# Optimization experiments

Hardware: AMD Instinct MI355X
Metric: run time of the kernel (lower is better)

Reference implementation:

```python
import jax, jax.numpy as jnp
import numpy as np

N_NODES = 50000
IN_CH = 32
HID = 64
N_EDGES = 800000
B = 4


def setup_inputs() -> dict:
    key = jax.random.key(0)
    ks = jax.random.split(key, 20)
    inp = {
        "x": jax.random.normal(ks[0], (B, N_NODES, IN_CH), dtype=jnp.float32),
        "h": jax.random.normal(ks[1], (B, N_NODES, HID), dtype=jnp.float32),
        "edge_index": jax.random.randint(ks[2], (2, N_EDGES), 0, N_NODES, dtype=jnp.int64),
        "edge_weight": jax.random.uniform(ks[3], (N_EDGES,), dtype=jnp.float32),
    }
    # 6 GCNConv layers: uz, hz, ur, hr, uh, hh. W stored as [in, out]; bias [out].
    names = [("uz", IN_CH), ("hz", HID), ("ur", IN_CH), ("hr", HID), ("uh", IN_CH), ("hh", HID)]
    for i, (nm, cin) in enumerate(names):
        scale = 1.0 / np.sqrt(cin)
        inp[f"W_{nm}"] = jax.random.uniform(ks[4 + 2 * i], (cin, HID), minval=-scale, maxval=scale, dtype=jnp.float32)
        inp[f"b_{nm}"] = jax.random.uniform(ks[5 + 2 * i], (HID,), minval=-scale, maxval=scale, dtype=jnp.float32)
    return inp


def _gcn_norm(edge_index, edge_weight, n):
    # add self-loops with weight 1, symmetric normalization (PyG GCNConv default)
    loop = jnp.arange(n, dtype=edge_index.dtype)
    src = jnp.concatenate([edge_index[0], loop])
    dst = jnp.concatenate([edge_index[1], loop])
    w = jnp.concatenate([edge_weight, jnp.ones((n,), edge_weight.dtype)])
    deg = jnp.zeros((n,), edge_weight.dtype).at[dst].add(w)
    dinv = jnp.where(deg > 0, jax.lax.rsqrt(jnp.maximum(deg, 1e-12)), 0.0)
    norm = dinv[src] * w * dinv[dst]
    return src, dst, norm


def _gcn(x, W, b, src, dst, norm, n):
    # x: [B, N, Cin] -> [B, N, H]; linear then normalized scatter-add over edges
    xw = jnp.einsum("bnc,ch->bnh", x, W)
    msg = xw[:, src, :] * norm[None, :, None]          # [B, E+N, H]
    agg = jnp.zeros((x.shape[0], n, W.shape[1]), x.dtype).at[:, dst].add(msg)
    return agg + b


def reference(x, h, edge_index, edge_weight,
              W_uz, b_uz, W_hz, b_hz, W_ur, b_ur, W_hr, b_hr, W_uh, b_uh, W_hh, b_hh):
    n = x.shape[1]
    src, dst, norm = _gcn_norm(edge_index, edge_weight, n)
    z = jax.nn.sigmoid(_gcn(x, W_uz, b_uz, src, dst, norm, n)
                       + _gcn(h, W_hz, b_hz, src, dst, norm, n))
    r = jax.nn.sigmoid(_gcn(x, W_ur, b_ur, src, dst, norm, n)
                       + _gcn(h, W_hr, b_hr, src, dst, norm, n))
    h_hat = jnp.tanh(_gcn(x, W_uh, b_uh, src, dst, norm, n)
                     + _gcn(r * h, W_hh, b_hh, src, dst, norm, n))
    return (1.0 - z) * h + z * h_hat
```

## Files before the change

### kernel.cpp

```cpp
#include <hip/hip_runtime.h>
#include <math.h>

#define NN 50000
#define CIN 32
#define HD  64
#define NE  800000
#define NB  4
#define NBLK 196
#define NTILE 12500
#define TPB   3125
#define DWAVES 2048

typedef unsigned int uint32;
typedef unsigned short ushort_t;
typedef unsigned long long u64;
typedef __attribute__((ext_vector_type(8))) short bf16x8;
typedef __attribute__((ext_vector_type(4))) float f32x4;

__device__ __forceinline__ uint32 pk2(float a, float b) {
    uint32 ua = __float_as_uint(a), ub = __float_as_uint(b);
    uint32 ra = (ua + 0x7FFFu + ((ua >> 16) & 1u)) >> 16;
    uint32 rb = (ub + 0x7FFFu + ((ub >> 16) & 1u)) >> 16;
    return ra | (rb << 16);
}
__device__ __forceinline__ ushort_t b1(float v) {
    uint32 u = __float_as_uint(v);
    return (ushort_t)((u + 0x7FFFu + ((u >> 16) & 1u)) >> 16);
}
__device__ __forceinline__ float ub(ushort_t v) {
    return __uint_as_float(((uint32)v) << 16);
}
__device__ __forceinline__ float blo(uint32 v) { return __uint_as_float(v << 16); }
__device__ __forceinline__ float bhi(uint32 v) { return __uint_as_float(v & 0xFFFF0000u); }
__device__ __forceinline__ float sigm(float v) { return 1.0f / (1.0f + __expf(-v)); }


__global__ void k_prep(const float* __restrict__ x, const float* __restrict__ h,
                       const float* __restrict__ Wuz, const float* __restrict__ Whz,
                       const float* __restrict__ Wur, const float* __restrict__ Whr,
                       const float* __restrict__ Wuh, const float* __restrict__ Whh,
                       const float* __restrict__ buz, const float* __restrict__ bhz,
                       const float* __restrict__ bur, const float* __restrict__ bhr,
                       const float* __restrict__ buh, const float* __restrict__ bhh,
                       uint32* __restrict__ F, u64* __restrict__ degcnt,
                       uint32* __restrict__ WB, float* __restrict__ BS) {
    int stride = gridDim.x * blockDim.x;
    int tid = blockIdx.x * blockDim.x + threadIdx.x;

    if (tid < NN) degcnt[tid] = (1ull << 24);

    if (tid < 9216) {
        int g = tid / 3072, rem = tid - g * 3072;
        int kt = rem >> 10, r2 = rem & 1023;
        int ct = r2 >> 8, r3 = r2 & 255;
        int l = r3 >> 2, jp = r3 & 3;
        int k = kt * 32 + ((l >> 4) << 3) + 2 * jp;
        int ch = ct * 16 + (l & 15);
        const float* Wu = (g == 0) ? Wuz : (g == 1) ? Wur : Wuh;
        const float* Wh = (g == 0) ? Whz : (g == 1) ? Whr : Whh;
        float w0 = (k < 32) ? Wu[k * 64 + ch] : Wh[(k - 32) * 64 + ch];
        int k1 = k + 1;
        float w1 = (k1 < 32) ? Wu[k1 * 64 + ch] : Wh[(k1 - 32) * 64 + ch];
        WB[tid] = pk2(w0, w1);
    }
    if (tid < 192) {
        int g = tid >> 6, c = tid & 63;
        const float* bu = (g == 0) ? buz : (g == 1) ? bur : buh;
        const float* bh = (g == 0) ? bhz : (g == 1) ? bhr : bhh;
        BS[tid] = bu[c] + bh[c];
    }

    for (int t = tid; t < NB * NN * (CIN / 2); t += stride) {
        int cp = t & 15; int rest = t >> 4;
        int b = rest / NN; int n = rest - b * NN;
        float2 v = *(const float2*)&x[(b * NN + n) * CIN + 2 * cp];
        F[n * 192 + b * 16 + cp] = pk2(v.x, v.y);
    }
    for (int t = tid; t < NB * NN * (HD / 2); t += stride) {
        int cp = t & 31; int rest = t >> 5;
        int b = rest / NN; int n = rest - b * NN;
        float2 v = *(const float2*)&h[(b * NN + n) * HD + 2 * cp];
        F[n * 192 + 64 + b * 32 + cp] = pk2(v.x, v.y);
    }
}

__global__ void k_degcnt(const int* __restrict__ ei, const float* __restrict__ ew,
                         u64* __restrict__ degcnt) {
    int stride = gridDim.x * blockDim.x;
    for (int e = blockIdx.x * blockDim.x + threadIdx.x; e < NE; e += stride) {
        int d = ei[NE + e];
        u64 val = (1ull << 40) + (u64)(uint32)(ew[e] * 16777216.0f + 0.5f);
        atomicAdd(&degcnt[d], val);
    }
}


__global__ void k_scan1(const u64* __restrict__ degcnt, int* __restrict__ tmp,
                        int* __restrict__ partials) {
    __shared__ int lds[256];
    int i = blockIdx.x * 256 + threadIdx.x;
    int v = (i < NN) ? (int)(degcnt[i] >> 40) : 0;
    lds[threadIdx.x] = v;
    __syncthreads();
    for (int off = 1; off < 256; off <<= 1) {
        int t = (threadIdx.x >= off) ? lds[threadIdx.x - off] : 0;
        __syncthreads();
        lds[threadIdx.x] += t;
        __syncthreads();
    }
    if (i < NN) tmp[i] = lds[threadIdx.x];
    if (threadIdx.x == 255) partials[blockIdx.x] = lds[255];
}

__global__ void k_scan2(int* __restrict__ partials) {
    __shared__ int lds[256];
    int v = (threadIdx.x < NBLK) ? partials[threadIdx.x] : 0;
    lds[threadIdx.x] = v;
    __syncthreads();
    for (int off = 1; off < 256; off <<= 1) {
        int t = (threadIdx.x >= off) ? lds[threadIdx.x - off] : 0;
        __syncthreads();
        lds[threadIdx.x] += t;
        __syncthreads();
    }
    int ex = (threadIdx.x > 0) ? lds[threadIdx.x - 1] : 0;
    if (threadIdx.x < NBLK) partials[threadIdx.x] = ex;
}

__global__ void k_scan3(const int* __restrict__ tmp, const u64* __restrict__ degcnt,
                        const int* __restrict__ partials,
                        int* __restrict__ rowptr, int* __restrict__ cursor,
                        float* __restrict__ dinv) {
    int i = blockIdx.x * blockDim.x + threadIdx.x;
    if (i < NN) {
        u64 dc = degcnt[i];
        int cnt = (int)(dc >> 40);
        int inc = tmp[i] + partials[i >> 8];
        rowptr[i + 1] = inc;
        cursor[i] = inc - cnt;
        if (i == 0) rowptr[0] = 0;
        float dg = (float)(dc & 0xFFFFFFFFFFull) * 5.9604644775390625e-08f;
        dinv[i] = (dg > 0.0f) ? rsqrtf(fmaxf(dg, 1e-12f)) : 0.0f;
    }
}

__global__ void k_bucket(const int* __restrict__ ei, const float* __restrict__ ew,
                         const float* __restrict__ dinv,
                         int* __restrict__ cursor, int2* __restrict__ eb) {
    int stride = gridDim.x * blockDim.x;
    for (int e = blockIdx.x * blockDim.x + threadIdx.x; e < NE; e += stride) {
        int s = ei[e], d = ei[NE + e];
        float nrm = dinv[s] * ew[e] * dinv[d];
        int pos = atomicAdd(&cursor[d], 1);
        eb[pos] = make_int2(s, __float_as_int(nrm));
    }
}


__global__ __launch_bounds__(256) void k_gather_xh(
    const int* __restrict__ rowptr, const int2* __restrict__ eb,
    const float* __restrict__ dinv, const uint32* __restrict__ F,
    uint32* __restrict__ AggU) {

    int l = threadIdx.x & 63;
    int d = __builtin_amdgcn_readfirstlane(blockIdx.x * 4 + (threadIdx.x >> 6));
    float dv = dinv[d];
    float s2 = dv * dv;

    const uint32* fp = F + 3 * l;
    const uint32* sp = fp + d * 192;
    uint32 u0 = sp[0], u1 = sp[1], u2 = sp[2];
    float a0 = s2 * blo(u0), a1 = s2 * bhi(u0);
    float a2 = s2 * blo(u1), a3 = s2 * bhi(u1);
    float a4 = s2 * blo(u2), a5 = s2 * bhi(u2);

    int e  = rowptr[d];
    int e1 = rowptr[d + 1];

    for (; e + 7 < e1; e += 8) {
        int2 p0 = eb[e],     p1 = eb[e + 1], p2 = eb[e + 2], p3 = eb[e + 3];
        int2 p4 = eb[e + 4], p5 = eb[e + 5], p6 = eb[e + 6], p7 = eb[e + 7];
        const uint32* q0 = fp + p0.x * 192;
        const uint32* q1 = fp + p1.x * 192;
        const uint32* q2 = fp + p2.x * 192;
        const uint32* q3 = fp + p3.x * 192;
        const uint32* q4 = fp + p4.x * 192;
        const uint32* q5 = fp + p5.x * 192;
        const uint32* q6 = fp + p6.x * 192;
        const uint32* q7 = fp + p7.x * 192;
        uint32 v00 = q0[0], v01 = q0[1], v02 = q0[2];
        uint32 v10 = q1[0], v11 = q1[1], v12 = q1[2];
        uint32 v20 = q2[0], v21 = q2[1], v22 = q2[2];
        uint32 v30 = q3[0], v31 = q3[1], v32 = q3[2];
        uint32 v40 = q4[0], v41 = q4[1], v42 = q4[2];
        uint32 v50 = q5[0], v51 = q5[1], v52 = q5[2];
        uint32 v60 = q6[0], v61 = q6[1], v62 = q6[2];
        uint32 v70 = q7[0], v71 = q7[1], v72 = q7[2];
        float n0 = __int_as_float(p0.y), n1 = __int_as_float(p1.y);
        float n2 = __int_as_float(p2.y), n3 = __int_as_float(p3.y);
        float n4 = __int_as_float(p4.y), n5 = __int_as_float(p5.y);
        float n6 = __int_as_float(p6.y), n7 = __int_as_float(p7.y);
        a0 = fmaf(n0, blo(v00), a0); a1 = fmaf(n0, bhi(v00), a1);
        a2 = fmaf(n0, blo(v01), a2); a3 = fmaf(n0, bhi(v01), a3);
        a4 = fmaf(n0, blo(v02), a4); a5 = fmaf(n0, bhi(v02), a5);
        a0 = fmaf(n1, blo(v10), a0); a1 = fmaf(n1, bhi(v10), a1);
        a2 = fmaf(n1, blo(v11), a2); a3 = fmaf(n1, bhi(v11), a3);
        a4 = fmaf(n1, blo(v12), a4); a5 = fmaf(n1, bhi(v12), a5);
        a0 = fmaf(n2, blo(v20), a0); a1 = fmaf(n2, bhi(v20), a1);
        a2 = fmaf(n2, blo(v21), a2); a3 = fmaf(n2, bhi(v21), a3);
        a4 = fmaf(n2, blo(v22), a4); a5 = fmaf(n2, bhi(v22), a5);
        a0 = fmaf(n3, blo(v30), a0); a1 = fmaf(n3, bhi(v30), a1);
        a2 = fmaf(n3, blo(v31), a2); a3 = fmaf(n3, bhi(v31), a3);
        a4 = fmaf(n3, blo(v32), a4); a5 = fmaf(n3, bhi(v32), a5);
        a0 = fmaf(n4, blo(v40), a0); a1 = fmaf(n4, bhi(v40), a1);
        a2 = fmaf(n4, blo(v41), a2); a3 = fmaf(n4, bhi(v41), a3);
        a4 = fmaf(n4, blo(v42), a4); a5 = fmaf(n4, bhi(v42), a5);
        a0 = fmaf(n5, blo(v50), a0); a1 = fmaf(n5, bhi(v50), a1);
        a2 = fmaf(n5, blo(v51), a2); a3 = fmaf(n5, bhi(v51), a3);
        a4 = fmaf(n5, blo(v52), a4); a5 = fmaf(n5, bhi(v52), a5);
        a0 = fmaf(n6, blo(v60), a0); a1 = fmaf(n6, bhi(v60), a1);
        a2 = fmaf(n6, blo(v61), a2); a3 = fmaf(n6, bhi(v61), a3);
        a4 = fmaf(n6, blo(v62), a4); a5 = fmaf(n6, bhi(v62), a5);
        a0 = fmaf(n7, blo(v70), a0); a1 = fmaf(n7, bhi(v70), a1);
        a2 = fmaf(n7, blo(v71), a2); a3 = fmaf(n7, bhi(v71), a3);
        a4 = fmaf(n7, blo(v72), a4); a5 = fmaf(n7, bhi(v72), a5);
    }
    for (; e + 3 < e1; e += 4) {
        int2 p0 = eb[e], p1 = eb[e + 1], p2 = eb[e + 2], p3 = eb[e + 3];
        const uint32* q0 = fp + p0.x * 192;
        const uint32* q1 = fp + p1.x * 192;
        const uint32* q2 = fp + p2.x * 192;
        const uint32* q3 = fp + p3.x * 192;
        uint32 v00 = q0[0], v01 = q0[1], v02 = q0[2];
        uint32 v10 = q1[0], v11 = q1[1], v12 = q1[2];
        uint32 v20 = q2[0], v21 = q2[1], v22 = q2[2];
        uint32 v30 = q3[0], v31 = q3[1], v32 = q3[2];
        float n0 = __int_as_float(p0.y), n1 = __int_as_float(p1.y);
        float n2 = __int_as_float(p2.y), n3 = __int_as_float(p3.y);
        a0 = fmaf(n0, blo(v00), a0); a1 = fmaf(n0, bhi(v00), a1);
        a2 = fmaf(n0, blo(v01), a2); a3 = fmaf(n0, bhi(v01), a3);
        a4 = fmaf(n0, blo(v02), a4); a5 = fmaf(n0, bhi(v02), a5);
        a0 = fmaf(n1, blo(v10), a0); a1 = fmaf(n1, bhi(v10), a1);
        a2 = fmaf(n1, blo(v11), a2); a3 = fmaf(n1, bhi(v11), a3);
        a4 = fmaf(n1, blo(v12), a4); a5 = fmaf(n1, bhi(v12), a5);
        a0 = fmaf(n2, blo(v20), a0); a1 = fmaf(n2, bhi(v20), a1);
        a2 = fmaf(n2, blo(v21), a2); a3 = fmaf(n2, bhi(v21), a3);
        a4 = fmaf(n2, blo(v22), a4); a5 = fmaf(n2, bhi(v22), a5);
        a0 = fmaf(n3, blo(v30), a0); a1 = fmaf(n3, bhi(v30), a1);
        a2 = fmaf(n3, blo(v31), a2); a3 = fmaf(n3, bhi(v31), a3);
        a4 = fmaf(n3, blo(v32), a4); a5 = fmaf(n3, bhi(v32), a5);
    }
    for (; e < e1; ++e) {
        int2 p0 = eb[e];
        const uint32* q0 = fp + p0.x * 192;
        uint32 v00 = q0[0], v01 = q0[1], v02 = q0[2];
        float n0 = __int_as_float(p0.y);
        a0 = fmaf(n0, blo(v00), a0); a1 = fmaf(n0, bhi(v00), a1);
        a2 = fmaf(n0, blo(v01), a2); a3 = fmaf(n0, bhi(v01), a3);
        a4 = fmaf(n0, blo(v02), a4); a5 = fmaf(n0, bhi(v02), a5);
    }

    uint32* op = AggU + d * 192 + 3 * l;
    op[0] = pk2(a0, a1);
    op[1] = pk2(a2, a3);
    op[2] = pk2(a4, a5);
}

__global__ __launch_bounds__(256) void k_gather_rh(
    const int* __restrict__ rowptr, const int2* __restrict__ eb,
    const float* __restrict__ dinv, const uint32* __restrict__ R,
    uint32* __restrict__ AggU) {

    int l = threadIdx.x & 63;
    int d = __builtin_amdgcn_readfirstlane(blockIdx.x * 4 + (threadIdx.x >> 6));
    float dv = dinv[d];
    float s2 = dv * dv;

    const uint32* rp = R + 2 * l;
    uint2 sv = *(const uint2*)(rp + d * 128);
    float a0 = s2 * blo(sv.x), a1 = s2 * bhi(sv.x);
    float a2 = s2 * blo(sv.y), a3 = s2 * bhi(sv.y);

    int e  = rowptr[d];
    int e1 = rowptr[d + 1];

    for (; e + 7 < e1; e += 8) {
        int2 p0 = eb[e],     p1 = eb[e + 1], p2 = eb[e + 2], p3 = eb[e + 3];
        int2 p4 = eb[e + 4], p5 = eb[e + 5], p6 = eb[e + 6], p7 = eb[e + 7];
        uint2 v0 = *(const uint2*)(rp + p0.x * 128);
        uint2 v1 = *(const uint2*)(rp + p1.x * 128);
        uint2 v2 = *(const uint2*)(rp + p2.x * 128);
        uint2 v3 = *(const uint2*)(rp + p3.x * 128);
        uint2 v4 = *(const uint2*)(rp + p4.x * 128);
        uint2 v5 = *(const uint2*)(rp + p5.x * 128);
        uint2 v6 = *(const uint2*)(rp + p6.x * 128);
        uint2 v7 = *(const uint2*)(rp + p7.x * 128);
        float n0 = __int_as_float(p0.y), n1 = __int_as_float(p1.y);
        float n2 = __int_as_float(p2.y), n3 = __int_as_float(p3.y);
        float n4 = __int_as_float(p4.y), n5 = __int_as_float(p5.y);
        float n6 = __int_as_float(p6.y), n7 = __int_as_float(p7.y);
        a0 = fmaf(n0, blo(v0.x), a0); a1 = fmaf(n0, bhi(v0.x), a1);
        a2 = fmaf(n0, blo(v0.y), a2); a3 = fmaf(n0, bhi(v0.y), a3);
        a0 = fmaf(n1, blo(v1.x), a0); a1 = fmaf(n1, bhi(v1.x), a1);
        a2 = fmaf(n1, blo(v1.y), a2); a3 = fmaf(n1, bhi(v1.y), a3);
        a0 = fmaf(n2, blo(v2.x), a0); a1 = fmaf(n2, bhi(v2.x), a1);
        a2 = fmaf(n2, blo(v2.y), a2); a3 = fmaf(n2, bhi(v2.y), a3);
        a0 = fmaf(n3, blo(v3.x), a0); a1 = fmaf(n3, bhi(v3.x), a1);
        a2 = fmaf(n3, blo(v3.y), a2); a3 = fmaf(n3, bhi(v3.y), a3);
        a0 = fmaf(n4, blo(v4.x), a0); a1 = fmaf(n4, bhi(v4.x), a1);
        a2 = fmaf(n4, blo(v4.y), a2); a3 = fmaf(n4, bhi(v4.y), a3);
        a0 = fmaf(n5, blo(v5.x), a0); a1 = fmaf(n5, bhi(v5.x), a1);
        a2 = fmaf(n5, blo(v5.y), a2); a3 = fmaf(n5, bhi(v5.y), a3);
        a0 = fmaf(n6, blo(v6.x), a0); a1 = fmaf(n6, bhi(v6.x), a1);
        a2 = fmaf(n6, blo(v6.y), a2); a3 = fmaf(n6, bhi(v6.y), a3);
        a0 = fmaf(n7, blo(v7.x), a0); a1 = fmaf(n7, bhi(v7.x), a1);
        a2 = fmaf(n7, blo(v7.y), a2); a3 = fmaf(n7, bhi(v7.y), a3);
    }
    for (; e + 3 < e1; e += 4) {
        int2 p0 = eb[e], p1 = eb[e + 1], p2 = eb[e + 2], p3 = eb[e + 3];
        uint2 v0 = *(const uint2*)(rp + p0.x * 128);
        uint2 v1 = *(const uint2*)(rp + p1.x * 128);
        uint2 v2 = *(const uint2*)(rp + p2.x * 128);
        uint2 v3 = *(const uint2*)(rp + p3.x * 128);
        float n0 = __int_as_float(p0.y), n1 = __int_as_float(p1.y);
        float n2 = __int_as_float(p2.y), n3 = __int_as_float(p3.y);
        a0 = fmaf(n0, blo(v0.x), a0); a1 = fmaf(n0, bhi(v0.x), a1);
        a2 = fmaf(n0, blo(v0.y), a2); a3 = fmaf(n0, bhi(v0.y), a3);
        a0 = fmaf(n1, blo(v1.x), a0); a1 = fmaf(n1, bhi(v1.x), a1);
        a2 = fmaf(n1, blo(v1.y), a2); a3 = fmaf(n1, bhi(v1.y), a3);
        a0 = fmaf(n2, blo(v2.x), a0); a1 = fmaf(n2, bhi(v2.x), a1);
        a2 = fmaf(n2, blo(v2.y), a2); a3 = fmaf(n2, bhi(v2.y), a3);
        a0 = fmaf(n3, blo(v3.x), a0); a1 = fmaf(n3, bhi(v3.x), a1);
        a2 = fmaf(n3, blo(v3.y), a2); a3 = fmaf(n3, bhi(v3.y), a3);
    }
    for (; e < e1; ++e) {
        int2 p0 = eb[e];
        uint2 v0 = *(const uint2*)(rp + p0.x * 128);
        float n0 = __int_as_float(p0.y);
        a0 = fmaf(n0, blo(v0.x), a0); a1 = fmaf(n0, bhi(v0.x), a1);
        a2 = fmaf(n0, blo(v0.y), a2); a3 = fmaf(n0, bhi(v0.y), a3);
    }

    *(uint2*)&AggU[d * 192 + 64 + (l >> 4) * 32 + ((2 * l) & 31)] =
        make_uint2(pk2(a0, a1), pk2(a2, a3));
}


__global__ __launch_bounds__(256) void k_zr(
    const uint32* __restrict__ AggU, const float* __restrict__ h,
    const uint32* __restrict__ WB, const float* __restrict__ BS,
    ushort_t* __restrict__ Zb, ushort_t* __restrict__ R16) {

    int l  = threadIdx.x & 63;
    int wv = blockIdx.x * 4 + (threadIdx.x >> 6);
    int lr = l & 15, lg = l >> 4;

    const bf16x8* wz = (const bf16x8*)WB;
    const bf16x8* wr = (const bf16x8*)(WB + 3072);
    bf16x8 wzf[12], wrf[12];
    #pragma unroll
    for (int f = 0; f < 12; ++f) { wzf[f] = wz[f * 64 + l]; wrf[f] = wr[f * 64 + l]; }
    float bz[4], br[4];
    #pragma unroll
    for (int ct = 0; ct < 4; ++ct) {
        bz[ct] = BS[ct * 16 + lr];
        br[ct] = BS[64 + ct * 16 + lr];
    }

    for (int t = wv; t < NTILE; t += DWAVES) {
        int bb = t / TPB, nt = t - bb * TPB;
        const uint32* base = AggU + (nt * 16 + lr) * 192;
        bf16x8 af0 = *(const bf16x8*)(base + bb * 16 + lg * 4);
        bf16x8 af1 = *(const bf16x8*)(base + 64 + bb * 32 + lg * 4);
        bf16x8 af2 = *(const bf16x8*)(base + 64 + bb * 32 + 16 + lg * 4);

        f32x4 az[4], ar[4];
        #pragma unroll
        for (int c = 0; c < 4; ++c) { az[c] = (f32x4){0,0,0,0}; ar[c] = (f32x4){0,0,0,0}; }

        #pragma unroll
        for (int ct = 0; ct < 4; ++ct) {
            az[ct] = __builtin_amdgcn_mfma_f32_16x16x32_bf16(af0, wzf[0*4+ct], az[ct], 0,0,0);
            ar[ct] = __builtin_amdgcn_mfma_f32_16x16x32_bf16(af0, wrf[0*4+ct], ar[ct], 0,0,0);
            az[ct] = __builtin_amdgcn_mfma_f32_16x16x32_bf16(af1, wzf[1*4+ct], az[ct], 0,0,0);
            ar[ct] = __builtin_amdgcn_mfma_f32_16x16x32_bf16(af1, wrf[1*4+ct], ar[ct], 0,0,0);
            az[ct] = __builtin_amdgcn_mfma_f32_16x16x32_bf16(af2, wzf[2*4+ct], az[ct], 0,0,0);
            ar[ct] = __builtin_amdgcn_mfma_f32_16x16x32_bf16(af2, wrf[2*4+ct], ar[ct], 0,0,0);
        }

        int node0 = nt * 16;
        #pragma unroll
        for (int ct = 0; ct < 4; ++ct) {
            int ch = ct * 16 + lr;
            #pragma unroll
            for (int rr = 0; rr < 4; ++rr) {
                int node = node0 + lg * 4 + rr;
                int off  = (bb * NN + node) * 64 + ch;
                float zv = sigm(az[ct][rr] + bz[ct]);
                float rv = sigm(ar[ct][rr] + br[ct]);
                float hv = h[off];
                Zb[off] = b1(zv);
                R16[node * 256 + bb * 64 + ch] = b1(rv * hv);
            }
        }
    }
}

__global__ __launch_bounds__(256) void k_final(
    const uint32* __restrict__ AggU, const float* __restrict__ h,
    const uint32* __restrict__ WB, const float* __restrict__ BS,
    const ushort_t* __restrict__ Zb, float* __restrict__ out) {

    int l  = threadIdx.x & 63;
    int wv = blockIdx.x * 4 + (threadIdx.x >> 6);
    int lr = l & 15, lg = l >> 4;

    const bf16x8* wh = (const bf16x8*)(WB + 6144);
    bf16x8 whf[12];
    #pragma unroll
    for (int f = 0; f < 12; ++f) whf[f] = wh[f * 64 + l];
    float bs[4];
    #pragma unroll
    for (int ct = 0; ct < 4; ++ct) bs[ct] = BS[128 + ct * 16 + lr];

    for (int t = wv; t < NTILE; t += DWAVES) {
        int bb = t / TPB, nt = t - bb * TPB;
        const uint32* base = AggU + (nt * 16 + lr) * 192;
        bf16x8 af0 = *(const bf16x8*)(base + bb * 16 + lg * 4);
        bf16x8 af1 = *(const bf16x8*)(base + 64 + bb * 32 + lg * 4);
        bf16x8 af2 = *(const bf16x8*)(base + 64 + bb * 32 + 16 + lg * 4);

        f32x4 ac[4];
        #pragma unroll
        for (int c = 0; c < 4; ++c) ac[c] = (f32x4){0,0,0,0};

        #pragma unroll
        for (int ct = 0; ct < 4; ++ct) {
            ac[ct] = __builtin_amdgcn_mfma_f32_16x16x32_bf16(af0, whf[0*4+ct], ac[ct], 0,0,0);
            ac[ct] = __builtin_amdgcn_mfma_f32_16x16x32_bf16(af1, whf[1*4+ct], ac[ct], 0,0,0);
            ac[ct] = __builtin_amdgcn_mfma_f32_16x16x32_bf16(af2, whf[2*4+ct], ac[ct], 0,0,0);
        }

        int node0 = nt * 16;
        #pragma unroll
        for (int ct = 0; ct < 4; ++ct) {
            int ch = ct * 16 + lr;
            #pragma unroll
            for (int rr = 0; rr < 4; ++rr) {
                int node = node0 + lg * 4 + rr;
                int off  = (bb * NN + node) * 64 + ch;
                float hh = tanhf(ac[ct][rr] + bs[ct]);
                float zv = ub(Zb[off]);
                float hv = h[off];
                out[off] = (1.0f - zv) * hv + zv * hh;
            }
        }
    }
}


extern "C" void kernel_launch(void* const* d_in, const int* in_sizes, int n_in,
                              void* d_out, int out_size, void* d_ws, size_t ws_size,
                              hipStream_t stream) {
    const float* x   = (const float*)d_in[0];
    const float* h   = (const float*)d_in[1];
    const int*   ei  = (const int*)d_in[2];
    const float* ew  = (const float*)d_in[3];
    const float* Wuz = (const float*)d_in[4];
    const float* buz = (const float*)d_in[5];
    const float* Whz = (const float*)d_in[6];
    const float* bhz = (const float*)d_in[7];
    const float* Wur = (const float*)d_in[8];
    const float* bur = (const float*)d_in[9];
    const float* Whr = (const float*)d_in[10];
    const float* bhr = (const float*)d_in[11];
    const float* Wuh = (const float*)d_in[12];
    const float* buh = (const float*)d_in[13];
    const float* Whh = (const float*)d_in[14];
    const float* bhh = (const float*)d_in[15];
    float* out = (float*)d_out;

    float*    w      = (float*)d_ws;
    u64*      degcnt = (u64*)w;
    float*    dinv   = w + 102400;
    int*      rowptr = (int*)(w + 153600);
    int2*     eb     = (int2*)(w + 204800);
    uint32*   F      = (uint32*)(w + 1804800);
    uint32*   R      = F;
    uint32*   AggU   = (uint32*)(w + 11404800);
    ushort_t* Zb     = (ushort_t*)(w + 21004800);
    uint32*   WB     = (uint32*)(w + 27404800);
    float*    BS     = (float*)(w + 27414016);
    int*      tmp    = (int*)(w + 27414208);
    int*      cursor = (int*)(w + 27465408);
    int*      parts  = (int*)(w + 27516608);

    k_prep<<<2048, 256, 0, stream>>>(x, h,
                                     Wuz, Whz, Wur, Whr, Wuh, Whh,
                                     buz, bhz, bur, bhr, buh, bhh,
                                     F, degcnt, WB, BS);
    k_degcnt<<<2048, 256, 0, stream>>>(ei, ew, degcnt);

    k_scan1<<<NBLK, 256, 0, stream>>>(degcnt, tmp, parts);
    k_scan2<<<1, 256, 0, stream>>>(parts);
    k_scan3<<<NBLK, 256, 0, stream>>>(tmp, degcnt, parts, rowptr, cursor, dinv);

    k_bucket<<<2048, 256, 0, stream>>>(ei, ew, dinv, cursor, eb);

    k_gather_xh<<<NN / 4, 256, 0, stream>>>(rowptr, eb, dinv, F, AggU);

    k_zr<<<DWAVES / 4, 256, 0, stream>>>(AggU, h, WB, BS, Zb, (ushort_t*)R);

    k_gather_rh<<<NN / 4, 256, 0, stream>>>(rowptr, eb, dinv, R, AggU);

    k_final<<<DWAVES / 4, 256, 0, stream>>>(AggU, h, WB, BS, Zb, out);
}
```

Baseline: 350.7 us.

## Vectorize prep packing, store Z in MFMA fragment order, read bf16 h copy

The prep kernel now reads x and h as float4 and writes two packed bf16 pairs per store. The z/r and final kernels read h from the bf16 packed feature buffer instead of fp32 global h, halving those reads. Z is stored as uint2 in the MFMA output-fragment order, so each lane writes and reads it with one 8-byte access instead of scattered 2-byte ones. The workspace is re-laid out so R no longer aliases F, because F must survive until k_final; using bf16 h in the final blend adds rounding error to the output.

```diff
diff --git a/kernel.cpp b/kernel.cpp
--- a/kernel.cpp
+++ b/kernel.cpp
@@ -23,26 +23,19 @@
     uint32 rb = (ub + 0x7FFFu + ((ub >> 16) & 1u)) >> 16;
     return ra | (rb << 16);
 }
-__device__ __forceinline__ ushort_t b1(float v) {
-    uint32 u = __float_as_uint(v);
-    return (ushort_t)((u + 0x7FFFu + ((u >> 16) & 1u)) >> 16);
-}
-__device__ __forceinline__ float ub(ushort_t v) {
-    return __uint_as_float(((uint32)v) << 16);
-}
 __device__ __forceinline__ float blo(uint32 v) { return __uint_as_float(v << 16); }
 __device__ __forceinline__ float bhi(uint32 v) { return __uint_as_float(v & 0xFFFF0000u); }
 __device__ __forceinline__ float sigm(float v) { return 1.0f / (1.0f + __expf(-v)); }
 
 
-__global__ void k_prep(const float* __restrict__ x, const float* __restrict__ h,
+__global__ void k_prep(const float4* __restrict__ x4, const float4* __restrict__ h4,
                        const float* __restrict__ Wuz, const float* __restrict__ Whz,
                        const float* __restrict__ Wur, const float* __restrict__ Whr,
                        const float* __restrict__ Wuh, const float* __restrict__ Whh,
                        const float* __restrict__ buz, const float* __restrict__ bhz,
                        const float* __restrict__ bur, const float* __restrict__ bhr,
                        const float* __restrict__ buh, const float* __restrict__ bhh,
-                       uint32* __restrict__ F, u64* __restrict__ degcnt,
+                       uint2* __restrict__ F2, u64* __restrict__ degcnt,
                        uint32* __restrict__ WB, float* __restrict__ BS) {
     int stride = gridDim.x * blockDim.x;
     int tid = blockIdx.x * blockDim.x + threadIdx.x;
@@ -70,17 +63,17 @@
         BS[tid] = bu[c] + bh[c];
     }
 
-    for (int t = tid; t < NB * NN * (CIN / 2); t += stride) {
-        int cp = t & 15; int rest = t >> 4;
+    for (int t = tid; t < NB * NN * (CIN / 4); t += stride) {
+        int cq = t & 7; int rest = t >> 3;
         int b = rest / NN; int n = rest - b * NN;
-        float2 v = *(const float2*)&x[(b * NN + n) * CIN + 2 * cp];
-        F[n * 192 + b * 16 + cp] = pk2(v.x, v.y);
-    }
-    for (int t = tid; t < NB * NN * (HD / 2); t += stride) {
-        int cp = t & 31; int rest = t >> 5;
+        float4 v = x4[(b * NN + n) * 8 + cq];
+        F2[n * 96 + b * 8 + cq] = make_uint2(pk2(v.x, v.y), pk2(v.z, v.w));
+    }
+    for (int t = tid; t < NB * NN * (HD / 4); t += stride) {
+        int cq = t & 15; int rest = t >> 4;
         int b = rest / NN; int n = rest - b * NN;
-        float2 v = *(const float2*)&h[(b * NN + n) * HD + 2 * cp];
-        F[n * 192 + 64 + b * 32 + cp] = pk2(v.x, v.y);
+        float4 v = h4[(b * NN + n) * 16 + cq];
+        F2[n * 96 + 32 + b * 16 + cq] = make_uint2(pk2(v.x, v.y), pk2(v.z, v.w));
     }
 }
 
@@ -347,9 +340,9 @@
 
 
 __global__ __launch_bounds__(256) void k_zr(
-    const uint32* __restrict__ AggU, const float* __restrict__ h,
+    const uint32* __restrict__ AggU, const uint32* __restrict__ F,
     const uint32* __restrict__ WB, const float* __restrict__ BS,
-    ushort_t* __restrict__ Zb, ushort_t* __restrict__ R16) {
+    uint2* __restrict__ Zb2, ushort_t* __restrict__ R16) {
 
     int l  = threadIdx.x & 63;
     int wv = blockIdx.x * 4 + (threadIdx.x >> 6);
@@ -392,24 +385,33 @@
         #pragma unroll
         for (int ct = 0; ct < 4; ++ct) {
             int ch = ct * 16 + lr;
+            uint32 z01, z23;
             #pragma unroll
             for (int rr = 0; rr < 4; ++rr) {
                 int node = node0 + lg * 4 + rr;
-                int off  = (bb * NN + node) * 64 + ch;
                 float zv = sigm(az[ct][rr] + bz[ct]);
                 float rv = sigm(ar[ct][rr] + br[ct]);
-                float hv = h[off];
-                Zb[off] = b1(zv);
-                R16[node * 256 + bb * 64 + ch] = b1(rv * hv);
+                uint32 hu = F[node * 192 + 64 + bb * 32 + ct * 8 + (lr >> 1)];
+                float hv = (lr & 1) ? bhi(hu) : blo(hu);
+                uint32 zb = (__float_as_uint(zv) + 0x7FFFu + ((__float_as_uint(zv) >> 16) & 1u)) >> 16;
+                if (rr == 0) z01 = zb;
+                else if (rr == 1) z01 |= zb << 16;
+                else if (rr == 2) z23 = zb;
+                else z23 |= zb << 16;
+                float rh = rv * hv;
+                uint32 ru = __float_as_uint(rh);
+                R16[node * 256 + bb * 64 + ch] =
+                    (ushort_t)((ru + 0x7FFFu + ((ru >> 16) & 1u)) >> 16);
             }
+            Zb2[(t * 4 + ct) * 64 + l] = make_uint2(z01, z23);
         }
     }
 }
 
 __global__ __launch_bounds__(256) void k_final(
-    const uint32* __restrict__ AggU, const float* __restrict__ h,
+    const uint32* __restrict__ AggU, const uint32* __restrict__ F,
     const uint32* __restrict__ WB, const float* __restrict__ BS,
-    const ushort_t* __restrict__ Zb, float* __restrict__ out) {
+    const uint2* __restrict__ Zb2, float* __restrict__ out) {
 
     int l  = threadIdx.x & 63;
     int wv = blockIdx.x * 4 + (threadIdx.x >> 6);
@@ -445,13 +447,16 @@
         #pragma unroll
         for (int ct = 0; ct < 4; ++ct) {
             int ch = ct * 16 + lr;
+            uint2 zv2 = Zb2[(t * 4 + ct) * 64 + l];
             #pragma unroll
             for (int rr = 0; rr < 4; ++rr) {
                 int node = node0 + lg * 4 + rr;
                 int off  = (bb * NN + node) * 64 + ch;
                 float hh = tanhf(ac[ct][rr] + bs[ct]);
-                float zv = ub(Zb[off]);
-                float hv = h[off];
+                float zv = (rr == 0) ? blo(zv2.x) : (rr == 1) ? bhi(zv2.x)
+                         : (rr == 2) ? blo(zv2.y) : bhi(zv2.y);
+                uint32 hu = F[node * 192 + 64 + bb * 32 + ct * 8 + (lr >> 1)];
+                float hv = (lr & 1) ? bhi(hu) : blo(hu);
                 out[off] = (1.0f - zv) * hv + zv * hh;
             }
         }
@@ -482,23 +487,23 @@
 
     float*    w      = (float*)d_ws;
     u64*      degcnt = (u64*)w;
-    float*    dinv   = w + 102400;
-    int*      rowptr = (int*)(w + 153600);
-    int2*     eb     = (int2*)(w + 204800);
-    uint32*   F      = (uint32*)(w + 1804800);
-    uint32*   R      = F;
-    uint32*   AggU   = (uint32*)(w + 11404800);
-    ushort_t* Zb     = (ushort_t*)(w + 21004800);
-    uint32*   WB     = (uint32*)(w + 27404800);
-    float*    BS     = (float*)(w + 27414016);
-    int*      tmp    = (int*)(w + 27414208);
-    int*      cursor = (int*)(w + 27465408);
-    int*      parts  = (int*)(w + 27516608);
-
-    k_prep<<<2048, 256, 0, stream>>>(x, h,
+    int*      tmp    = (int*)(w + 102400);
+    int*      cursor = (int*)(w + 153600);
+    int*      parts  = (int*)(w + 204800);
+    uint2*    Zb2    = (uint2*)w;
+    float*    dinv   = w + 6400000;
+    int*      rowptr = (int*)(w + 6451200);
+    int2*     eb     = (int2*)(w + 6502400);
+    uint32*   F      = (uint32*)(w + 8102400);
+    uint32*   AggU   = (uint32*)(w + 17702400);
+    uint32*   R      = (uint32*)(w + 27302400);
+    uint32*   WB     = (uint32*)(w + 33702400);
+    float*    BS     = (float*)(w + 33711616);
+
+    k_prep<<<2048, 256, 0, stream>>>((const float4*)x, (const float4*)h,
                                      Wuz, Whz, Wur, Whr, Wuh, Whh,
                                      buz, bhz, bur, bhr, buh, bhh,
-                                     F, degcnt, WB, BS);
+                                     (uint2*)F, degcnt, WB, BS);
     k_degcnt<<<2048, 256, 0, stream>>>(ei, ew, degcnt);
 
     k_scan1<<<NBLK, 256, 0, stream>>>(degcnt, tmp, parts);
@@ -509,9 +514,9 @@
 
     k_gather_xh<<<NN / 4, 256, 0, stream>>>(rowptr, eb, dinv, F, AggU);
 
-    k_zr<<<DWAVES / 4, 256, 0, stream>>>(AggU, h, WB, BS, Zb, (ushort_t*)R);
+    k_zr<<<DWAVES / 4, 256, 0, stream>>>(AggU, F, WB, BS, Zb2, (ushort_t*)R);
 
     k_gather_rh<<<NN / 4, 256, 0, stream>>>(rowptr, eb, dinv, R, AggU);
 
-    k_final<<<DWAVES / 4, 256, 0, stream>>>(AggU, h, WB, BS, Zb, out);
-}
+    k_final<<<DWAVES / 4, 256, 0, stream>>>(AggU, F, WB, BS, Zb2, out);
+}
```

After: 332.7 us. 1.05x faster.
